# Optimization experiments

Hardware: AMD Instinct MI355X
Metric: run time of the kernel (lower is better)

## Reference

```python
import jax, jax.numpy as jnp
import numpy as np

B, S, D, K = 4, 4096, 1024, 64

def setup_inputs() -> dict:
    key = jax.random.key(0)
    kx, kq, kk, kv, ko = jax.random.split(key, 5)
    scale = 1.0 / np.sqrt(D)
    return {
        "x": jax.random.normal(kx, (B, S, D), dtype=jnp.float32),
        "Wq": jax.random.uniform(kq, (K, D), dtype=jnp.float32, minval=-scale, maxval=scale),
        "Wk": jax.random.uniform(kk, (K, D), dtype=jnp.float32, minval=-scale, maxval=scale),
        "Wv": jax.random.uniform(kv, (K, D), dtype=jnp.float32, minval=-scale, maxval=scale),
        "Wo": jax.random.uniform(ko, (D, K), dtype=jnp.float32, minval=-1.0/np.sqrt(K), maxval=1.0/np.sqrt(K)),
    }

def reference(x, Wq, Wk, Wv, Wo):
    # projections: torch Linear(dim, key_dim, bias=False) -> x @ W.T
    Q = jax.nn.elu(x @ Wq.T) + 1.0          # [B,S,K]
    Kf = jax.nn.elu(x @ Wk.T) + 1.0         # [B,S,K]
    V = x @ Wv.T                             # [B,S,K]
    # causal running KV state via cumsum of outer products: [B,S,K,K]
    KV_sum = jnp.cumsum(Kf[..., :, None] * V[..., None, :], axis=1)
    K_sum = jnp.cumsum(Kf, axis=1)           # [B,S,K]
    num = jnp.einsum('bsk,bskm->bsm', Q, KV_sum)   # [B,S,K]
    den = jnp.einsum('bsk,bsk->bs', Q, K_sum)[..., None]
    out = num / (den + 1e-6)
    return out @ Wo.T                         # [B,S,D]
```

## Files before the change

### kernel.cpp

```cpp
#include <hip/hip_runtime.h>

#define BB 4
#define SS 4096
#define DDIM 1024
#define KDIM 64
#define NCHUNK 64
#define TCHUNK 256
#define MROWS 16384

typedef short short8v __attribute__((ext_vector_type(8)));
typedef float f32x4 __attribute__((ext_vector_type(4)));
#define MFMA16 __builtin_amdgcn_mfma_f32_16x16x32_bf16

#define GLDS16(gp, lp) __builtin_amdgcn_global_load_lds( \
    (const __attribute__((address_space(1))) unsigned int*)(gp), \
    (__attribute__((address_space(3))) unsigned int*)(lp), 16, 0, 0)

__device__ __forceinline__ ushort f2bf(float f) {
    uint u = __float_as_uint(f);
    u += 0x7FFFu + ((u >> 16) & 1u);
    return (ushort)(u >> 16);
}

__device__ __forceinline__ uint cvtpk(float lo, float hi) {
    uint r;
    asm("v_cvt_pk_bf16_f32 %0, %1, %2" : "=v"(r) : "v"(lo), "v"(hi));
    return r;
}

__global__ __launch_bounds__(256) void k_wconv(
    const float* __restrict__ Wq, const float* __restrict__ Wk,
    const float* __restrict__ Wv, const float* __restrict__ Wo,
    ushort* __restrict__ Whf, ushort* __restrict__ Wof)
{
    const int b = blockIdx.x, t = threadIdx.x;
    const int ks = t >> 7;
    const int l = (t >> 1) & 63;
    const int half = t & 1;
    if (b < 192) {
        const int s = b / 12, cf = b % 12;
        const int grow = cf * 16 + (l & 15);
        const int gcol = s * 64 + ks * 32 + ((l >> 4) & 3) * 8 + half * 4;
        const float* src = (grow < 64) ? (Wq + (size_t)grow * DDIM)
                         : (grow < 128) ? (Wk + (size_t)(grow - 64) * DDIM)
                                        : (Wv + (size_t)(grow - 128) * DDIM);
        float4 v = *(const float4*)&src[gcol];
        ushort* dst = &Whf[(size_t)(((s * 12 + cf) * 2 + ks) * 64 + l) * 8 + half * 4];
        dst[0] = f2bf(v.x); dst[1] = f2bf(v.y); dst[2] = f2bf(v.z); dst[3] = f2bf(v.w);
    } else {
        const int cf = b - 192;
        const int d = cf * 16 + (l & 15);
        const int kc = ks * 32 + ((l >> 4) & 3) * 8 + half * 4;
        float4 v = *(const float4*)&Wo[(size_t)d * KDIM + kc];
        ushort* dst = &Wof[(size_t)((cf * 2 + ks) * 64 + l) * 8 + half * 4];
        dst[0] = f2bf(v.x); dst[1] = f2bf(v.y); dst[2] = f2bf(v.z); dst[3] = f2bf(v.w);
    }
}

#define EBP 216
__global__ __launch_bounds__(512, 2) void k_proj(
    const float* __restrict__ x, const ushort* __restrict__ Whf,
    ushort* __restrict__ Qf, ushort* __restrict__ Kff,
    ushort* __restrict__ KfT, ushort* __restrict__ VT)
{
    __shared__ ushort lds[2][14336];
    const int t = threadIdx.x;
    const int w = t >> 6, l = t & 63;
    const int rw = w >> 2, cw = w & 3;
    const int mb = blockIdx.x;
    const int row0 = mb * 32;
    const int lq = l >> 4;

    const int xr = t >> 4;
    const int xc = (t & 15) * 4;
    const float* xbase = &x[(size_t)(row0 + xr) * DDIM + xc];
    const int xslot = (((xr >> 4) * 2 + (xc >> 5)) * 64
                       + ((xr & 15) | (((xc >> 3) & 3) << 4))) * 8 + ((xc >> 2) & 1) * 4;

    auto ldX = [&](int s) -> float4 { return *(const float4*)(xbase + s * 64); };
    auto stX = [&](float4 v, int buf) {
        uint2 pk;
        pk.x = cvtpk(v.x, v.y);
        pk.y = cvtpk(v.z, v.w);
        *(uint2*)&lds[buf][xslot] = pk;
    };
    auto stageW = [&](int s, int buf) {
#pragma unroll
        for (int ii = 0; ii < 3; ++ii) {
            const int f = w * 3 + ii;
            const ushort* gp = &Whf[(size_t)(s * 24 + f) * 512 + l * 8];
            GLDS16(gp, &lds[buf][2048 + f * 512]);
        }
    };

    f32x4 acc[3];
#pragma unroll
    for (int c = 0; c < 3; ++c) acc[c] = (f32x4){0.f, 0.f, 0.f, 0.f};

    auto compute = [&](int buf) {
#pragma unroll
        for (int ks = 0; ks < 2; ++ks) {
            short8v a = *(const short8v*)&lds[buf][((rw * 2 + ks) * 64 + l) * 8];
#pragma unroll
            for (int c = 0; c < 3; ++c) {
                short8v b = *(const short8v*)&lds[buf][2048 + ((cw * 3 + c) * 2 + ks) * 512 + l * 8];
                acc[c] = MFMA16(a, b, acc[c], 0, 0, 0);
            }
        }
    };

    float4 xe = ldX(0);
    float4 xo = ldX(1);
    stX(xe, 0);
    stageW(0, 0);
    asm volatile("s_waitcnt vmcnt(0) lgkmcnt(0)" ::: "memory");
    __builtin_amdgcn_s_barrier();
    __builtin_amdgcn_sched_barrier(0);

#pragma unroll
    for (int s = 0; s < 16; ++s) {
        const int cur = s & 1, nxt = cur ^ 1;
        stageW((s + 1) & 15, nxt);
        if ((s & 1) == 0) xe = ldX((s + 2) & 15);
        else              xo = ldX((s + 2) & 15);
        asm volatile("s_waitcnt vmcnt(5)" ::: "memory");
        __builtin_amdgcn_sched_barrier(0);
        compute(cur);
        stX((s & 1) == 0 ? xo : xe, nxt);
        asm volatile("s_waitcnt lgkmcnt(0)" ::: "memory");
        __builtin_amdgcn_s_barrier();
        __builtin_amdgcn_sched_barrier(0);
    }

    __syncthreads();

    ushort* eb = &lds[0][0];
#pragma unroll
    for (int c = 0; c < 3; ++c) {
        const int col = (cw * 3 + c) * 16 + (l & 15);
#pragma unroll
        for (int q = 0; q < 4; ++q) {
            const int row = rw * 16 + lq * 4 + q;
            float v = acc[c][q];
            if (col < 128) v = (v > 0.f) ? v + 1.f : __expf(v);
            eb[row * EBP + col] = f2bf(v);
        }
    }
    __syncthreads();

    {
        const int which = w >> 2, rf = (w >> 1) & 1, ks = w & 1;
        const int r = rf * 16 + (l & 15);
        const int c0 = ks * 32 + ((l >> 4) & 3) * 8 + (which ? 64 : 0);
        short8v v8 = *(const short8v*)&eb[r * EBP + c0];
        const size_t fo = ((size_t)(mb * 4 + rf * 2 + ks)) * 512 + l * 8;
        if (which == 0) *(short8v*)&Qf[fo] = v8;
        else            *(short8v*)&Kff[fo] = v8;
    }
    {
        const int which = w >> 2, f = w & 3;
        const int col = (which ? 128 : 64) + f * 16 + (l & 15);
        const int jb = ((l >> 4) & 3) * 8;
        short8v tv;
#pragma unroll
        for (int e = 0; e < 8; ++e) tv[e] = (short)eb[(jb + e) * EBP + col];
        const size_t fo = ((size_t)((mb >> 1) * 8 + f * 2 + (mb & 1))) * 512 + l * 8;
        if (which == 0) *(short8v*)&KfT[fo] = tv;
        else            *(short8v*)&VT[fo]  = tv;
    }
}

__global__ __launch_bounds__(64) void k_chunksum(
    const ushort* __restrict__ KfT, const ushort* __restrict__ VT,
    float* __restrict__ KVc, float* __restrict__ Ksc)
{
    const int g = blockIdx.x, l = threadIdx.x;
    short8v ka[4][2], vb[4][2];
#pragma unroll
    for (int f = 0; f < 4; ++f)
#pragma unroll
        for (int js = 0; js < 2; ++js) {
            const size_t fo = ((size_t)(g * 8 + f * 2 + js)) * 512 + l * 8;
            ka[f][js] = *(const short8v*)&KfT[fo];
            vb[f][js] = *(const short8v*)&VT[fo];
        }
    short8v onesf;
#pragma unroll
    for (int e = 0; e < 8; ++e) onesf[e] = ((l & 15) == 0) ? (short)0x3F80 : (short)0;

    f32x4 acc[4][5];
#pragma unroll
    for (int kf = 0; kf < 4; ++kf)
#pragma unroll
        for (int mf = 0; mf < 5; ++mf) acc[kf][mf] = (f32x4){0.f, 0.f, 0.f, 0.f};
#pragma unroll
    for (int js = 0; js < 2; ++js)
#pragma unroll
        for (int kf = 0; kf < 4; ++kf) {
#pragma unroll
            for (int mf = 0; mf < 4; ++mf)
                acc[kf][mf] = MFMA16(ka[kf][js], vb[mf][js], acc[kf][mf], 0, 0, 0);
            acc[kf][4] = MFMA16(ka[kf][js], onesf, acc[kf][4], 0, 0, 0);
        }
    const int lq = l >> 4;
#pragma unroll
    for (int kf = 0; kf < 4; ++kf) {
#pragma unroll
        for (int q = 0; q < 4; ++q) {
            const int k = kf * 16 + lq * 4 + q;
#pragma unroll
            for (int mf = 0; mf < 4; ++mf)
                KVc[(size_t)g * 4096 + k * 64 + mf * 16 + (l & 15)] = acc[kf][mf][q];
            if ((l & 15) == 0) Ksc[(size_t)g * KDIM + k] = acc[kf][4][q];
        }
    }
}

__global__ void k_scan(const float* __restrict__ KVc, const float* __restrict__ Ksc,
                       float* __restrict__ Sst, float* __restrict__ Kss)
{
    const int b = blockIdx.x / 65;
    const int r = blockIdx.x % 65;
    const int t = threadIdx.x;
    if (r < 64) {
        const int e = r * 64 + t;
        float v[64];
#pragma unroll
        for (int i = 0; i < 64; ++i)
            v[i] = KVc[((size_t)(b * NCHUNK + i)) * 4096 + e];
        float acc = 0.f;
#pragma unroll
        for (int i = 0; i < 64; ++i) {
            Sst[((size_t)(b * NCHUNK + i)) * 4096 + e] = acc;
            acc += v[i];
        }
    } else {
        float v[64];
#pragma unroll
        for (int i = 0; i < 64; ++i)
            v[i] = Ksc[((size_t)(b * NCHUNK + i)) * KDIM + t];
        float acc = 0.f;
#pragma unroll
        for (int i = 0; i < 64; ++i) {
            Kss[((size_t)(b * NCHUNK + i)) * KDIM + t] = acc;
            acc += v[i];
        }
    }
}

__global__ __launch_bounds__(256) void k_intra(
    const ushort* __restrict__ Qf, const ushort* __restrict__ Kff,
    const ushort* __restrict__ VT, const float* __restrict__ Sst,
    const float* __restrict__ Kss, const ushort* __restrict__ Wof,
    float* __restrict__ out)
{
    __shared__ ushort pb[32 * 64];
    __shared__ ushort sT[80 * 64];
    __shared__ float ob[4][16 * 68 + 4];
    const int bx = blockIdx.x, t = threadIdx.x;
    const int g = bx >> 1, rh = bx & 1;
    const int w = t >> 6, l = t & 63;
    const int lq = l >> 4;

    {
        const int k = t >> 2, m0 = (t & 3) * 16;
        const float4* sp = (const float4*)&Sst[(size_t)g * 4096 + k * 64 + m0];
        float4 f0 = sp[0], f1 = sp[1], f2v = sp[2], f3 = sp[3];
        float fv[16] = {f0.x, f0.y, f0.z, f0.w, f1.x, f1.y, f1.z, f1.w,
                        f2v.x, f2v.y, f2v.z, f2v.w, f3.x, f3.y, f3.z, f3.w};
#pragma unroll
        for (int i = 0; i < 16; ++i) {
            const int m = m0 + i;
            sT[m * 64 + (k ^ ((m & 7) << 3))] = f2bf(fv[i]);
        }
        if (t < 64) sT[64 * 64 + t] = f2bf(Kss[(size_t)g * KDIM + t]);
        for (int idx = t; idx < 960; idx += 256) sT[65 * 64 + idx] = 0;
    }

    const int rf = w & 1;
    short8v qa[2];
#pragma unroll
    for (int ks = 0; ks < 2; ++ks)
        qa[ks] = *(const short8v*)&Qf[((size_t)((g * 2 + rh) * 4 + rf * 2 + ks)) * 512 + l * 8];
    {
        const int cfh = w >> 1;
        f32x4 accs[2];
#pragma unroll
        for (int ci = 0; ci < 2; ++ci) accs[ci] = (f32x4){0.f, 0.f, 0.f, 0.f};
#pragma unroll
        for (int ci = 0; ci < 2; ++ci) {
            const int cf = cfh * 2 + ci;
#pragma unroll
            for (int ks = 0; ks < 2; ++ks) {
                short8v kb = *(const short8v*)&Kff[((size_t)((g * 2 + (cf >> 1)) * 4 + (cf & 1) * 2 + ks)) * 512 + l * 8];
                accs[ci] = MFMA16(qa[ks], kb, accs[ci], 0, 0, 0);
            }
        }
#pragma unroll
        for (int ci = 0; ci < 2; ++ci)
#pragma unroll
            for (int q = 0; q < 4; ++q) {
                const int row = rf * 16 + lq * 4 + q;
                const int col = (cfh * 2 + ci) * 16 + (l & 15);
                const float sv = (col <= rh * 32 + row) ? accs[ci][q] : 0.f;
                pb[row * 64 + (col ^ ((row & 7) << 3))] = f2bf(sv);
            }
    }
    __syncthreads();

    const int mg = w >> 1;
    f32x4 an0 = (f32x4){0.f,0.f,0.f,0.f}, an1 = (f32x4){0.f,0.f,0.f,0.f};
    f32x4 ad = (f32x4){0.f,0.f,0.f,0.f};
    short8v onesf;
#pragma unroll
    for (int e = 0; e < 8; ++e) onesf[e] = ((l & 15) == 0) ? (short)0x3F80 : (short)0;
#pragma unroll
    for (int js = 0; js < 2; ++js) {
        const int prow = rf * 16 + (l & 15);
        const int pbase = js * 32 + ((l >> 4) & 3) * 8;
        short8v pa = *(const short8v*)&pb[prow * 64 + (pbase ^ ((prow & 7) << 3))];
        short8v v0 = *(const short8v*)&VT[((size_t)(g * 8 + (mg * 2 + 0) * 2 + js)) * 512 + l * 8];
        short8v v1 = *(const short8v*)&VT[((size_t)(g * 8 + (mg * 2 + 1) * 2 + js)) * 512 + l * 8];
        an0 = MFMA16(pa, v0, an0, 0, 0, 0);
        an1 = MFMA16(pa, v1, an1, 0, 0, 0);
        ad  = MFMA16(pa, onesf, ad, 0, 0, 0);
    }
#pragma unroll
    for (int ks = 0; ks < 2; ++ks) {
        const int base = ks * 32 + ((l >> 4) & 3) * 8;
        const int r0 = (mg * 2 + 0) * 16 + (l & 15);
        const int r1 = (mg * 2 + 1) * 16 + (l & 15);
        const int r4 = 64 + (l & 15);
        short8v s0 = *(const short8v*)&sT[r0 * 64 + (base ^ ((r0 & 7) << 3))];
        short8v s1 = *(const short8v*)&sT[r1 * 64 + (base ^ ((r1 & 7) << 3))];
        short8v s4 = *(const short8v*)&sT[r4 * 64 + (base ^ ((r4 & 7) << 3))];
        an0 = MFMA16(qa[ks], s0, an0, 0, 0, 0);
        an1 = MFMA16(qa[ks], s1, an1, 0, 0, 0);
        ad  = MFMA16(qa[ks], s4, ad, 0, 0, 0);
    }
#pragma unroll
    for (int q = 0; q < 4; ++q) {
        const float den = __shfl(ad[q], (l & 48));
        const float rinv = 1.f / (den + 1e-6f);
        const int row = rf * 16 + lq * 4 + q;
        const int c0 = (mg * 2 + 0) * 16 + (l & 15);
        const int c1 = (mg * 2 + 1) * 16 + (l & 15);
        pb[row * 64 + (c0 ^ ((row & 7) << 3))] = f2bf(an0[q] * rinv);
        pb[row * 64 + (c1 ^ ((row & 7) << 3))] = f2bf(an1[q] * rinv);
    }
    __syncthreads();

    short8v oa[2][2];
#pragma unroll
    for (int rfi = 0; rfi < 2; ++rfi)
#pragma unroll
        for (int ks = 0; ks < 2; ++ks) {
            const int row = rfi * 16 + (l & 15);
            const int base = ks * 32 + ((l >> 4) & 3) * 8;
            oa[rfi][ks] = *(const short8v*)&pb[row * 64 + (base ^ ((row & 7) << 3))];
        }
    float* obw = ob[w];
#pragma unroll
    for (int rr = 0; rr < 4; ++rr) {
        f32x4 acco[2][4];
#pragma unroll
        for (int rfi = 0; rfi < 2; ++rfi)
#pragma unroll
            for (int ci = 0; ci < 4; ++ci) acco[rfi][ci] = (f32x4){0.f, 0.f, 0.f, 0.f};
#pragma unroll
        for (int ci = 0; ci < 4; ++ci) {
            const int cfg = w * 16 + rr * 4 + ci;
#pragma unroll
            for (int ks = 0; ks < 2; ++ks) {
                short8v wb = *(const short8v*)&Wof[((size_t)(cfg * 2 + ks)) * 512 + l * 8];
#pragma unroll
                for (int rfi = 0; rfi < 2; ++rfi)
                    acco[rfi][ci] = MFMA16(oa[rfi][ks], wb, acco[rfi][ci], 0, 0, 0);
            }
        }
#pragma unroll
        for (int rfi = 0; rfi < 2; ++rfi) {
#pragma unroll
            for (int ci = 0; ci < 4; ++ci)
#pragma unroll
                for (int q = 0; q < 4; ++q)
                    obw[(lq * 4 + q) * 68 + ci * 16 + (l & 15)] = acco[rfi][ci][q];
#pragma unroll
            for (int rg = 0; rg < 4; ++rg) {
                const int row = rg * 4 + lq;
                float4 vv = *(const float4*)&obw[row * 68 + (l & 15) * 4];
                *(float4*)&out[((size_t)(g * 64 + rh * 32 + rfi * 16 + row)) * DDIM
                               + w * 256 + rr * 64 + (l & 15) * 4] = vv;
            }
        }
    }
}

extern "C" void kernel_launch(void* const* d_in, const int* in_sizes, int n_in,
                              void* d_out, int out_size, void* d_ws, size_t ws_size,
                              hipStream_t stream)
{
    const float* x  = (const float*)d_in[0];
    const float* Wq = (const float*)d_in[1];
    const float* Wk = (const float*)d_in[2];
    const float* Wv = (const float*)d_in[3];
    const float* Wo = (const float*)d_in[4];
    float* out = (float*)d_out;

    float* ws   = (float*)d_ws;
    float* KVc  = ws;
    float* Sst  = KVc + (size_t)TCHUNK * 4096;
    float* Ksc  = Sst + (size_t)TCHUNK * 4096;
    float* Kss  = Ksc + (size_t)TCHUNK * KDIM;
    ushort* Whf = (ushort*)(Kss + (size_t)TCHUNK * KDIM);
    ushort* Wof = Whf + (size_t)192 * DDIM;
    ushort* Qf  = Wof + (size_t)64 * 1024;
    ushort* Kff = Qf  + (size_t)512 * 4 * 512;
    ushort* KfT = Kff + (size_t)512 * 4 * 512;
    ushort* VT  = KfT + (size_t)256 * 8 * 512;

    k_wconv<<<dim3(256), dim3(256), 0, stream>>>(Wq, Wk, Wv, Wo, Whf, Wof);
    k_proj<<<dim3(MROWS / 32), dim3(512), 0, stream>>>(x, Whf, Qf, Kff, KfT, VT);
    k_chunksum<<<dim3(TCHUNK), dim3(64), 0, stream>>>(KfT, VT, KVc, Ksc);
    k_scan<<<dim3(BB * 65), dim3(64), 0, stream>>>(KVc, Ksc, Sst, Kss);
    k_intra<<<dim3(TCHUNK * 2), dim3(256), 0, stream>>>(Qf, Kff, VT, Sst, Kss, Wof, out);
}
```

Measured before the change: 52.46 us.

## Fuse per-chunk KV outer-product sums into projection kernel epilogue

Removes the separate chunk-sum kernel. Each projection block now computes partial KV and K-sum state for its 32 rows with MFMA from LDS-staged transposed fragments, and writes half-chunk partials. The scan kernel adds the two partials per chunk before its prefix sum. This saves a launch and the KfT round trip through global memory. In exchange the partial buffers double in size, the scan does extra reads, and the projection kernel gains a sync and epilogue work.

```diff
diff --git a/kernel.cpp b/kernel.cpp
--- a/kernel.cpp
+++ b/kernel.cpp
@@ -60,8 +60,8 @@
 #define EBP 216
 __global__ __launch_bounds__(512, 2) void k_proj(
     const float* __restrict__ x, const ushort* __restrict__ Whf,
-    ushort* __restrict__ Qf, ushort* __restrict__ Kff,
-    ushort* __restrict__ KfT, ushort* __restrict__ VT)
+    ushort* __restrict__ Qf, ushort* __restrict__ Kff, ushort* __restrict__ VT,
+    float* __restrict__ KVp, float* __restrict__ KscP)
 {
     __shared__ ushort lds[2][14336];
     const int t = threadIdx.x;
@@ -157,6 +157,7 @@
         if (which == 0) *(short8v*)&Qf[fo] = v8;
         else            *(short8v*)&Kff[fo] = v8;
     }
+    ushort* tfr = &lds[1][0];
     {
         const int which = w >> 2, f = w & 3;
         const int col = (which ? 128 : 64) + f * 16 + (l & 15);
@@ -164,59 +165,35 @@
         short8v tv;
 #pragma unroll
         for (int e = 0; e < 8; ++e) tv[e] = (short)eb[(jb + e) * EBP + col];
-        const size_t fo = ((size_t)((mb >> 1) * 8 + f * 2 + (mb & 1))) * 512 + l * 8;
-        if (which == 0) *(short8v*)&KfT[fo] = tv;
-        else            *(short8v*)&VT[fo]  = tv;
-    }
-}
-
-__global__ __launch_bounds__(64) void k_chunksum(
-    const ushort* __restrict__ KfT, const ushort* __restrict__ VT,
-    float* __restrict__ KVc, float* __restrict__ Ksc)
-{
-    const int g = blockIdx.x, l = threadIdx.x;
-    short8v ka[4][2], vb[4][2];
-#pragma unroll
-    for (int f = 0; f < 4; ++f)
-#pragma unroll
-        for (int js = 0; js < 2; ++js) {
-            const size_t fo = ((size_t)(g * 8 + f * 2 + js)) * 512 + l * 8;
-            ka[f][js] = *(const short8v*)&KfT[fo];
-            vb[f][js] = *(const short8v*)&VT[fo];
-        }
-    short8v onesf;
-#pragma unroll
-    for (int e = 0; e < 8; ++e) onesf[e] = ((l & 15) == 0) ? (short)0x3F80 : (short)0;
-
-    f32x4 acc[4][5];
-#pragma unroll
-    for (int kf = 0; kf < 4; ++kf)
-#pragma unroll
-        for (int mf = 0; mf < 5; ++mf) acc[kf][mf] = (f32x4){0.f, 0.f, 0.f, 0.f};
-#pragma unroll
-    for (int js = 0; js < 2; ++js)
-#pragma unroll
-        for (int kf = 0; kf < 4; ++kf) {
-#pragma unroll
-            for (int mf = 0; mf < 4; ++mf)
-                acc[kf][mf] = MFMA16(ka[kf][js], vb[mf][js], acc[kf][mf], 0, 0, 0);
-            acc[kf][4] = MFMA16(ka[kf][js], onesf, acc[kf][4], 0, 0, 0);
-        }
-    const int lq = l >> 4;
-#pragma unroll
-    for (int kf = 0; kf < 4; ++kf) {
+        *(short8v*)&tfr[(size_t)w * 512 + l * 8] = tv;
+        if (which == 1)
+            *(short8v*)&VT[((size_t)((mb >> 1) * 8 + f * 2 + (mb & 1))) * 512 + l * 8] = tv;
+    }
+    __syncthreads();
+    {
+        const int kf = w & 3, mh = w >> 2;
+        short8v ka  = *(const short8v*)&tfr[(size_t)kf * 512 + l * 8];
+        short8v vb0 = *(const short8v*)&tfr[(size_t)(4 + mh * 2 + 0) * 512 + l * 8];
+        short8v vb1 = *(const short8v*)&tfr[(size_t)(4 + mh * 2 + 1) * 512 + l * 8];
+        f32x4 a0 = (f32x4){0.f,0.f,0.f,0.f}, a1 = (f32x4){0.f,0.f,0.f,0.f};
+        f32x4 adn = (f32x4){0.f,0.f,0.f,0.f};
+        a0 = MFMA16(ka, vb0, a0, 0, 0, 0);
+        a1 = MFMA16(ka, vb1, a1, 0, 0, 0);
+        short8v onesf;
+#pragma unroll
+        for (int e = 0; e < 8; ++e) onesf[e] = ((l & 15) == 0) ? (short)0x3F80 : (short)0;
+        if (mh == 0) adn = MFMA16(ka, onesf, adn, 0, 0, 0);
 #pragma unroll
         for (int q = 0; q < 4; ++q) {
             const int k = kf * 16 + lq * 4 + q;
-#pragma unroll
-            for (int mf = 0; mf < 4; ++mf)
-                KVc[(size_t)g * 4096 + k * 64 + mf * 16 + (l & 15)] = acc[kf][mf][q];
-            if ((l & 15) == 0) Ksc[(size_t)g * KDIM + k] = acc[kf][4][q];
-        }
-    }
-}
-
-__global__ void k_scan(const float* __restrict__ KVc, const float* __restrict__ Ksc,
+            KVp[(size_t)mb * 4096 + k * 64 + (mh * 2 + 0) * 16 + (l & 15)] = a0[q];
+            KVp[(size_t)mb * 4096 + k * 64 + (mh * 2 + 1) * 16 + (l & 15)] = a1[q];
+            if (mh == 0 && (l & 15) == 0) KscP[(size_t)mb * KDIM + k] = adn[q];
+        }
+    }
+}
+
+__global__ void k_scan(const float* __restrict__ KVp, const float* __restrict__ KscP,
                        float* __restrict__ Sst, float* __restrict__ Kss)
 {
     const int b = blockIdx.x / 65;
@@ -226,8 +203,10 @@
         const int e = r * 64 + t;
         float v[64];
 #pragma unroll
-        for (int i = 0; i < 64; ++i)
-            v[i] = KVc[((size_t)(b * NCHUNK + i)) * 4096 + e];
+        for (int i = 0; i < 64; ++i) {
+            const size_t g2 = (size_t)(b * NCHUNK + i) * 2;
+            v[i] = KVp[g2 * 4096 + e] + KVp[(g2 + 1) * 4096 + e];
+        }
         float acc = 0.f;
 #pragma unroll
         for (int i = 0; i < 64; ++i) {
@@ -237,8 +216,10 @@
     } else {
         float v[64];
 #pragma unroll
-        for (int i = 0; i < 64; ++i)
-            v[i] = Ksc[((size_t)(b * NCHUNK + i)) * KDIM + t];
+        for (int i = 0; i < 64; ++i) {
+            const size_t g2 = (size_t)(b * NCHUNK + i) * 2;
+            v[i] = KscP[g2 * KDIM + t] + KscP[(g2 + 1) * KDIM + t];
+        }
         float acc = 0.f;
 #pragma unroll
         for (int i = 0; i < 64; ++i) {
@@ -408,20 +389,18 @@
     float* out = (float*)d_out;
 
     float* ws   = (float*)d_ws;
-    float* KVc  = ws;
-    float* Sst  = KVc + (size_t)TCHUNK * 4096;
-    float* Ksc  = Sst + (size_t)TCHUNK * 4096;
-    float* Kss  = Ksc + (size_t)TCHUNK * KDIM;
+    float* KVp  = ws;
+    float* Sst  = KVp + (size_t)512 * 4096;
+    float* KscP = Sst + (size_t)TCHUNK * 4096;
+    float* Kss  = KscP + (size_t)512 * KDIM;
     ushort* Whf = (ushort*)(Kss + (size_t)TCHUNK * KDIM);
     ushort* Wof = Whf + (size_t)192 * DDIM;
     ushort* Qf  = Wof + (size_t)64 * 1024;
     ushort* Kff = Qf  + (size_t)512 * 4 * 512;
-    ushort* KfT = Kff + (size_t)512 * 4 * 512;
-    ushort* VT  = KfT + (size_t)256 * 8 * 512;
+    ushort* VT  = Kff + (size_t)512 * 4 * 512;
 
     k_wconv<<<dim3(256), dim3(256), 0, stream>>>(Wq, Wk, Wv, Wo, Whf, Wof);
-    k_proj<<<dim3(MROWS / 32), dim3(512), 0, stream>>>(x, Whf, Qf, Kff, KfT, VT);
-    k_chunksum<<<dim3(TCHUNK), dim3(64), 0, stream>>>(KfT, VT, KVc, Ksc);
-    k_scan<<<dim3(BB * 65), dim3(64), 0, stream>>>(KVc, Ksc, Sst, Kss);
+    k_proj<<<dim3(MROWS / 32), dim3(512), 0, stream>>>(x, Whf, Qf, Kff, VT, KVp, KscP);
+    k_scan<<<dim3(BB * 65), dim3(64), 0, stream>>>(KVp, KscP, Sst, Kss);
     k_intra<<<dim3(TCHUNK * 2), dim3(256), 0, stream>>>(Qf, Kff, VT, Sst, Kss, Wof, out);
 }
```

New measurement: 67.87 us. 1.29x slower.
